# Kernel tuning notes

Measured on AMD Instinct MI355X. Metric: run time of the kernel, lower is better.

Reference implementation:

```python
import jax, jax.numpy as jnp
import numpy as np

N_A = 50000   # 'user' nodes
N_B = 50000   # 'item' nodes
E = 1000000   # edges per relation
IN, HID, OUT = 128, 128, 64


def setup_inputs() -> dict:
    key = jax.random.key(0)
    ks = jax.random.split(key, 24)
    def glorot(k, shape):
        scale = 1.0 / np.sqrt(shape[0])
        return jax.random.normal(k, shape, jnp.float32) * scale
    inp = {
        "feat_A": jax.random.normal(ks[0], (N_A, IN), jnp.float32),
        "feat_B": jax.random.normal(ks[1], (N_B, IN), jnp.float32),
        "rates_src": jax.random.randint(ks[2], (E,), 0, N_A, jnp.int32),
        "rates_dst": jax.random.randint(ks[3], (E,), 0, N_B, jnp.int32),
        "ratedby_src": jax.random.randint(ks[4], (E,), 0, N_B, jnp.int32),
        "ratedby_dst": jax.random.randint(ks[5], (E,), 0, N_A, jnp.int32),
        "follows_src": jax.random.randint(ks[6], (E,), 0, N_A, jnp.int32),
        "follows_dst": jax.random.randint(ks[7], (E,), 0, N_A, jnp.int32),
        "neg_src": jax.random.randint(ks[8], (E,), 0, N_A, jnp.int32),
        "neg_dst": jax.random.randint(ks[9], (E,), 0, N_B, jnp.int32),
        "W1_rates": glorot(ks[10], (IN, HID)),   "b1_rates": jnp.zeros((HID,), jnp.float32),
        "W1_ratedby": glorot(ks[11], (IN, HID)), "b1_ratedby": jnp.zeros((HID,), jnp.float32),
        "W1_follows": glorot(ks[12], (IN, HID)), "b1_follows": jnp.zeros((HID,), jnp.float32),
        "W2_rates": glorot(ks[13], (HID, OUT)),   "b2_rates": jnp.zeros((OUT,), jnp.float32),
        "W2_ratedby": glorot(ks[14], (HID, OUT)), "b2_ratedby": jnp.zeros((OUT,), jnp.float32),
        "W2_follows": glorot(ks[15], (HID, OUT)), "b2_follows": jnp.zeros((OUT,), jnp.float32),
    }
    return inp


def _graph_conv(x_src, W, b, src, dst, n_src, n_dst):
    # DGL GraphConv, norm='both': D_dst^{-1/2} A D_src^{-1/2} (X W) + b
    ones = jnp.ones(src.shape[0], x_src.dtype)
    deg_out = jnp.maximum(jax.ops.segment_sum(ones, src, num_segments=n_src), 1.0)
    deg_in = jnp.maximum(jax.ops.segment_sum(ones, dst, num_segments=n_dst), 1.0)
    h = (x_src * (deg_out ** -0.5)[:, None]) @ W          # [n_src, d_out]
    agg = jax.ops.segment_sum(h[src], dst, num_segments=n_dst)  # SpMM
    return agg * (deg_in ** -0.5)[:, None] + b


def reference(feat_A, feat_B,
              W1_rates, b1_rates, W1_ratedby, b1_ratedby, W1_follows, b1_follows,
              W2_rates, b2_rates, W2_ratedby, b2_ratedby, W2_follows, b2_follows,
              rates_src, rates_dst, ratedby_src, ratedby_dst,
              follows_src, follows_dst, neg_src, neg_dst):
    # --- RGCN layer 1 (HeteroGraphConv, aggregate='sum') ---
    hB = _graph_conv(feat_A, W1_rates, b1_rates, rates_src, rates_dst, N_A, N_B)
    hA = (_graph_conv(feat_B, W1_ratedby, b1_ratedby, ratedby_src, ratedby_dst, N_B, N_A)
          + _graph_conv(feat_A, W1_follows, b1_follows, follows_src, follows_dst, N_A, N_A))
    hA = jax.nn.relu(hA)
    hB = jax.nn.relu(hB)
    # --- RGCN layer 2 ---
    oB = _graph_conv(hA, W2_rates, b2_rates, rates_src, rates_dst, N_A, N_B)
    oA = (_graph_conv(hB, W2_ratedby, b2_ratedby, ratedby_src, ratedby_dst, N_B, N_A)
          + _graph_conv(hA, W2_follows, b2_follows, follows_src, follows_dst, N_A, N_A))
    # --- HeteroInnerProduct (u_dot_v on etype 'rates') for pos and neg graphs ---
    pos_score = jnp.sum(oA[rates_src] * oB[rates_dst], axis=1, keepdims=True)  # [E, 1]
    neg_score = jnp.sum(oA[neg_src] * oB[neg_dst], axis=1, keepdims=True)      # [E, 1]
    return pos_score, neg_score
```

## Files before the change

kernel.cpp:

```cpp
#include <hip/hip_runtime.h>
#include <hip/hip_fp16.h>
#include <cstddef>
#include <type_traits>

#define N_NODES 50000
#define E_EDGES 1000000
#define NBUCK 196
#define ACHUNK 3907
#define MTILES 3125

typedef _Float16 f16x8 __attribute__((ext_vector_type(8)));
typedef float f32x4 __attribute__((ext_vector_type(4)));

__global__ __launch_bounds__(256) void bucket_hist(const int* __restrict__ i0, const int* __restrict__ i1,
                                                   const int* __restrict__ i2, const int* __restrict__ i3,
                                                   const int* __restrict__ i4, const int* __restrict__ i5,
                                                   int* __restrict__ bhist) {
    int arr = blockIdx.y;
    const int* idx = arr == 0 ? i0 : arr == 1 ? i1 : arr == 2 ? i2
                   : arr == 3 ? i3 : arr == 4 ? i4 : i5;
    __shared__ int l[NBUCK];
    for (int b = threadIdx.x; b < NBUCK; b += 256) l[b] = 0;
    __syncthreads();
    int e0 = blockIdx.x * ACHUNK;
    int e1 = e0 + ACHUNK; if (e1 > E_EDGES) e1 = E_EDGES;
    for (int i = e0 + threadIdx.x; i < e1; i += 256)
        atomicAdd(&l[((unsigned)idx[i]) >> 8], 1);
    __syncthreads();
    for (int b = threadIdx.x; b < NBUCK; b += 256)
        if (l[b]) atomicAdd(&bhist[arr * NBUCK + b], l[b]);
}

__global__ void bucket_scan2(const int* __restrict__ bhist, int* __restrict__ gbase,
                             int* __restrict__ gcur) {
    int arr = blockIdx.x;
    if (threadIdx.x == 0) {
        int run = 0;
        for (int b = 0; b < NBUCK; b++) {
            gbase[arr * (NBUCK + 1) + b] = run;
            gcur[arr * NBUCK + b] = run;
            run += bhist[arr * NBUCK + b];
        }
        gbase[arr * (NBUCK + 1) + NBUCK] = run;
    }
}

__global__ __launch_bounds__(256) void binP(const int* __restrict__ s0, const int* __restrict__ d0,
                                            const int* __restrict__ s1, const int* __restrict__ d1,
                                            const int* __restrict__ s2, const int* __restrict__ d2,
                                            int* __restrict__ gcur, unsigned* __restrict__ pairs) {
    int rel = blockIdx.y;
    int arr = 2 * rel + 1;
    const int* src = rel == 0 ? s0 : rel == 1 ? s1 : s2;
    const int* dst = rel == 0 ? d0 : rel == 1 ? d1 : d2;
    int e0 = blockIdx.x * ACHUNK;
    int e1 = e0 + ACHUNK; if (e1 > E_EDGES) e1 = E_EDGES;
    __shared__ int lcnt[NBUCK];
    __shared__ int lbase[NBUCK];
    for (int b = threadIdx.x; b < NBUCK; b += 256) lcnt[b] = 0;
    __syncthreads();
    for (int i = e0 + threadIdx.x; i < e1; i += 256)
        atomicAdd(&lcnt[((unsigned)dst[i]) >> 8], 1);
    __syncthreads();
    for (int b = threadIdx.x; b < NBUCK; b += 256) {
        lbase[b] = lcnt[b] ? atomicAdd(&gcur[arr * NBUCK + b], lcnt[b]) : 0;
        lcnt[b] = 0;
    }
    __syncthreads();
    unsigned* pp = pairs + (size_t)rel * E_EDGES;
    for (int i = e0 + threadIdx.x; i < e1; i += 256) {
        int d = dst[i];
        int b = ((unsigned)d) >> 8;
        int p = lbase[b] + atomicAdd(&lcnt[b], 1);
        pp[p] = ((unsigned)(d & 255) << 16) | (unsigned)src[i];
    }
}

__global__ __launch_bounds__(256) void binS(const int* __restrict__ s0, const int* __restrict__ s1,
                                            const int* __restrict__ s2,
                                            int* __restrict__ gcur, unsigned char* __restrict__ sbytes) {
    int rel = blockIdx.y;
    int arr = 2 * rel;
    const int* src = rel == 0 ? s0 : rel == 1 ? s1 : s2;
    int e0 = blockIdx.x * ACHUNK;
    int e1 = e0 + ACHUNK; if (e1 > E_EDGES) e1 = E_EDGES;
    __shared__ int lcnt[NBUCK];
    __shared__ int lbase[NBUCK];
    for (int b = threadIdx.x; b < NBUCK; b += 256) lcnt[b] = 0;
    __syncthreads();
    for (int i = e0 + threadIdx.x; i < e1; i += 256)
        atomicAdd(&lcnt[((unsigned)src[i]) >> 8], 1);
    __syncthreads();
    for (int b = threadIdx.x; b < NBUCK; b += 256) {
        lbase[b] = lcnt[b] ? atomicAdd(&gcur[arr * NBUCK + b], lcnt[b]) : 0;
        lcnt[b] = 0;
    }
    __syncthreads();
    unsigned char* sb = sbytes + (size_t)rel * E_EDGES;
    for (int i = e0 + threadIdx.x; i < e1; i += 256) {
        int s = src[i];
        int b = ((unsigned)s) >> 8;
        int p = lbase[b] + atomicAdd(&lcnt[b], 1);
        sb[p] = (unsigned char)(s & 255);
    }
}

__global__ __launch_bounds__(256) void countS(const unsigned char* __restrict__ sbytes,
                                              const int* __restrict__ gbase,
                                              float* __restrict__ scales) {
    int rel = blockIdx.y, b = blockIdx.x;
    int arr = 2 * rel;
    int p0 = gbase[arr * (NBUCK + 1) + b];
    int p1 = gbase[arr * (NBUCK + 1) + b + 1];
    const unsigned char* sb = sbytes + (size_t)rel * E_EDGES;
    __shared__ int cnt[256];
    cnt[threadIdx.x] = 0;
    __syncthreads();
    for (int i = p0 + threadIdx.x; i < p1; i += 256)
        atomicAdd(&cnt[sb[i]], 1);
    __syncthreads();
    int node = b * 256 + threadIdx.x;
    if (node < N_NODES) {
        int c = cnt[threadIdx.x];
        if (c < 1) c = 1;
        scales[(size_t)arr * N_NODES + node] = 1.0f / sqrtf((float)c);
    }
}

__global__ __launch_bounds__(256) void fillB2(const unsigned* __restrict__ pairs,
                                              const int* __restrict__ gbase,
                                              int* __restrict__ row_ptr,
                                              float* __restrict__ scales,
                                              int* __restrict__ col) {
    int rel = blockIdx.y, b = blockIdx.x;
    int arr = 2 * rel + 1;
    int gb = gbase[arr * (NBUCK + 1) + b];
    int ge = gbase[arr * (NBUCK + 1) + b + 1];
    const unsigned* pp = pairs + (size_t)rel * E_EDGES;
    __shared__ int cnt[256];
    __shared__ int rowbase[256];
    __shared__ int wsum[4];
    int t = threadIdx.x;
    cnt[t] = 0;
    __syncthreads();
    for (int i = gb + t; i < ge; i += 256)
        atomicAdd(&cnt[pp[i] >> 16], 1);
    __syncthreads();
    int lane = t & 63, wid = t >> 6;
    int c0 = cnt[t];
    int v = c0;
#pragma unroll
    for (int o = 1; o < 64; o <<= 1) {
        int u = __shfl_up(v, o);
        if (lane >= o) v += u;
    }
    if (lane == 63) wsum[wid] = v;
    __syncthreads();
    int base = gb;
    for (int w = 0; w < wid; w++) base += wsum[w];
    int excl = base + v - c0;
    rowbase[t] = excl;
    int node = b * 256 + t;
    if (node <= N_NODES)
        row_ptr[(size_t)rel * (N_NODES + 1) + node] = excl;
    if (node < N_NODES) {
        int c = c0; if (c < 1) c = 1;
        scales[(size_t)arr * N_NODES + node] = 1.0f / sqrtf((float)c);
    }
    cnt[t] = 0;
    __syncthreads();
    int* cl = col + (size_t)rel * E_EDGES;
    for (int i = gb + t; i < ge; i += 256) {
        unsigned p = pp[i];
        int dl = p >> 16;
        int slot = rowbase[dl] + atomicAdd(&cnt[dl], 1);
        cl[slot] = (int)(p & 0xFFFFu);
    }
}

__global__ void w_cvt6(const float* __restrict__ w0, const float* __restrict__ w1,
                       const float* __restrict__ w2, const float* __restrict__ w3,
                       const float* __restrict__ w4, const float* __restrict__ w5,
                       __half* __restrict__ t0, __half* __restrict__ t1,
                       __half* __restrict__ t2, __half* __restrict__ t3,
                       __half* __restrict__ t4, __half* __restrict__ t5) {
    int m = blockIdx.y;
    const float* W = m == 0 ? w0 : m == 1 ? w1 : m == 2 ? w2 : m == 3 ? w3 : m == 4 ? w4 : w5;
    __half* Wt = m == 0 ? t0 : m == 1 ? t1 : m == 2 ? t2 : m == 3 ? t3 : m == 4 ? t4 : t5;
    int ncol = m < 3 ? 128 : 64;
    int tot = 128 * ncol;
    for (int i = blockIdx.x * blockDim.x + threadIdx.x; i < tot; i += gridDim.x * blockDim.x) {
        int n = i >> 7, k = i & 127;
        Wt[i] = __float2half(W[k * ncol + n]);
    }
}

template <int NCOL, typename XT>
__global__ __launch_bounds__(256) void gemm_mfma(const XT* __restrict__ X,
                                                 const float* __restrict__ sc,
                                                 const __half* __restrict__ Wt,
                                                 __half* __restrict__ T) {
    constexpr int NHALF = NCOL / 64;
    int gw = (blockIdx.x * blockDim.x + threadIdx.x) >> 6;
    int lane = threadIdx.x & 63;
    int half_id = gw % NHALF;
    int mstream = gw / NHALF;
    int nstreams = ((gridDim.x * blockDim.x) >> 6) / NHALF;
    int l15 = lane & 15, g = lane >> 4;

    f16x8 b[4][4];
    {
        const __half* wb = Wt + ((size_t)half_id * 64 + l15) * 128 + g * 8;
#pragma unroll
        for (int nt = 0; nt < 4; nt++)
#pragma unroll
            for (int kb = 0; kb < 4; kb++)
                b[nt][kb] = *(const f16x8*)(wb + nt * 16 * 128 + kb * 32);
    }

    for (int mt = mstream; mt < MTILES; mt += nstreams) {
        int m0 = mt * 16;
        f16x8 a[4];
        if constexpr (std::is_same<XT, float>::value) {
            const float* xr = X + (size_t)(m0 + l15) * 128 + g * 8;
#pragma unroll
            for (int kb = 0; kb < 4; kb++) {
                float4 u = *(const float4*)(xr + kb * 32);
                float4 v = *(const float4*)(xr + kb * 32 + 4);
                f16x8 t;
                t[0] = (_Float16)u.x; t[1] = (_Float16)u.y;
                t[2] = (_Float16)u.z; t[3] = (_Float16)u.w;
                t[4] = (_Float16)v.x; t[5] = (_Float16)v.y;
                t[6] = (_Float16)v.z; t[7] = (_Float16)v.w;
                a[kb] = t;
            }
        } else {
            const _Float16* xr = (const _Float16*)X + (size_t)(m0 + l15) * 128 + g * 8;
#pragma unroll
            for (int kb = 0; kb < 4; kb++)
                a[kb] = *(const f16x8*)(xr + kb * 32);
        }
        f32x4 acc[4];
#pragma unroll
        for (int nt = 0; nt < 4; nt++) acc[nt] = (f32x4){0.f, 0.f, 0.f, 0.f};
#pragma unroll
        for (int kb = 0; kb < 4; kb++)
#pragma unroll
            for (int nt = 0; nt < 4; nt++)
                acc[nt] = __builtin_amdgcn_mfma_f32_16x16x32_f16(a[kb], b[nt][kb], acc[nt], 0, 0, 0);
        int mrow = m0 + g * 4;
#pragma unroll
        for (int j = 0; j < 4; j++) {
            float sj = sc[mrow + j];
            __half* tj = T + (size_t)(mrow + j) * NCOL + half_id * 64 + l15;
            tj[0]  = __float2half(acc[0][j] * sj);
            tj[16] = __float2half(acc[1][j] * sj);
            tj[32] = __float2half(acc[2][j] * sj);
            tj[48] = __float2half(acc[3][j] * sj);
        }
    }
}

template <bool ACCUM, bool RELU>
__global__ __launch_bounds__(256) void spmm128(const int* __restrict__ rp,
                                               const int* __restrict__ col,
                                               const __half* __restrict__ T,
                                               const float* __restrict__ s_in,
                                               const float* __restrict__ bias,
                                               __half* __restrict__ outp, int nrows) {
    int wave = (blockIdx.x * blockDim.x + threadIdx.x) >> 6;
    int lane = threadIdx.x & 63;
    int rowA = wave * 2, rowB = rowA + 1;
    if (rowA >= nrows) return;
    const char* Tb = (const char*)T;
    unsigned loff = (unsigned)lane << 2;
#define LD128(c) __half22float2(*(const __half2*)(Tb + (((unsigned)(c) << 8) + loff)))
    int begA = rp[rowA], endA = rp[rowA + 1];
    int eB = endA, endB = (rowB < nrows) ? rp[rowB + 1] : endA;
    float axA = 0.f, ayA = 0.f, axB = 0.f, ayB = 0.f;
    int eA = begA;
    while (eA + 4 <= endA && eB + 4 <= endB) {
        int a0 = col[eA], a1 = col[eA+1], a2 = col[eA+2], a3 = col[eA+3];
        int b0 = col[eB], b1 = col[eB+1], b2 = col[eB+2], b3 = col[eB+3];
        float2 va0 = LD128(a0), va1 = LD128(a1), va2 = LD128(a2), va3 = LD128(a3);
        float2 vb0 = LD128(b0), vb1 = LD128(b1), vb2 = LD128(b2), vb3 = LD128(b3);
        axA += (va0.x + va1.x) + (va2.x + va3.x);
        ayA += (va0.y + va1.y) + (va2.y + va3.y);
        axB += (vb0.x + vb1.x) + (vb2.x + vb3.x);
        ayB += (vb0.y + vb1.y) + (vb2.y + vb3.y);
        eA += 4; eB += 4;
    }
    while (eA + 4 <= endA) {
        int a0 = col[eA], a1 = col[eA+1], a2 = col[eA+2], a3 = col[eA+3];
        float2 va0 = LD128(a0), va1 = LD128(a1), va2 = LD128(a2), va3 = LD128(a3);
        axA += (va0.x + va1.x) + (va2.x + va3.x);
        ayA += (va0.y + va1.y) + (va2.y + va3.y);
        eA += 4;
    }
    while (eB + 4 <= endB) {
        int b0 = col[eB], b1 = col[eB+1], b2 = col[eB+2], b3 = col[eB+3];
        float2 vb0 = LD128(b0), vb1 = LD128(b1), vb2 = LD128(b2), vb3 = LD128(b3);
        axB += (vb0.x + vb1.x) + (vb2.x + vb3.x);
        ayB += (vb0.y + vb1.y) + (vb2.y + vb3.y);
        eB += 4;
    }
    while (eA < endA && eB < endB) {
        float2 va = LD128(col[eA]), vb = LD128(col[eB]);
        axA += va.x; ayA += va.y; axB += vb.x; ayB += vb.y;
        eA++; eB++;
    }
    for (; eA < endA; eA++) { float2 v = LD128(col[eA]); axA += v.x; ayA += v.y; }
    for (; eB < endB; eB++) { float2 v = LD128(col[eB]); axB += v.x; ayB += v.y; }
#undef LD128
    float bx = bias[2 * lane], by = bias[2 * lane + 1];
    {
        float s = s_in[rowA];
        __half2* po = (__half2*)(outp + (size_t)rowA * 128 + 2 * lane);
        float ox = fmaf(axA, s, bx), oy = fmaf(ayA, s, by);
        if constexpr (ACCUM) { float2 p = __half22float2(*po); ox += p.x; oy += p.y; }
        if constexpr (RELU) { ox = fmaxf(ox, 0.f); oy = fmaxf(oy, 0.f); }
        *po = __floats2half2_rn(ox, oy);
    }
    if (rowB < nrows) {
        float s = s_in[rowB];
        __half2* po = (__half2*)(outp + (size_t)rowB * 128 + 2 * lane);
        float ox = fmaf(axB, s, bx), oy = fmaf(ayB, s, by);
        if constexpr (ACCUM) { float2 p = __half22float2(*po); ox += p.x; oy += p.y; }
        if constexpr (RELU) { ox = fmaxf(ox, 0.f); oy = fmaxf(oy, 0.f); }
        *po = __floats2half2_rn(ox, oy);
    }
}

template <bool ACCUM>
__global__ __launch_bounds__(256) void spmm64(const int* __restrict__ rp,
                                              const int* __restrict__ col,
                                              const __half* __restrict__ T,
                                              const float* __restrict__ s_in,
                                              const float* __restrict__ bias,
                                              __half* __restrict__ outp, int nrows) {
    int g = (blockIdx.x * blockDim.x + threadIdx.x) >> 5;
    int l2 = threadIdx.x & 31;
    int rowA = g * 2, rowB = rowA + 1;
    if (rowA >= nrows) return;
    const char* Tb = (const char*)T;
    unsigned loff = (unsigned)l2 << 2;
#define LD64(c) __half22float2(*(const __half2*)(Tb + (((unsigned)(c) << 7) + loff)))
    int begA = rp[rowA], endA = rp[rowA + 1];
    int eB = endA, endB = (rowB < nrows) ? rp[rowB + 1] : endA;
    float axA = 0.f, ayA = 0.f, axB = 0.f, ayB = 0.f;
    int eA = begA;
    while (eA + 4 <= endA && eB + 4 <= endB) {
        int a0 = col[eA], a1 = col[eA+1], a2 = col[eA+2], a3 = col[eA+3];
        int b0 = col[eB], b1 = col[eB+1], b2 = col[eB+2], b3 = col[eB+3];
        float2 va0 = LD64(a0), va1 = LD64(a1), va2 = LD64(a2), va3 = LD64(a3);
        float2 vb0 = LD64(b0), vb1 = LD64(b1), vb2 = LD64(b2), vb3 = LD64(b3);
        axA += (va0.x + va1.x) + (va2.x + va3.x);
        ayA += (va0.y + va1.y) + (va2.y + va3.y);
        axB += (vb0.x + vb1.x) + (vb2.x + vb3.x);
        ayB += (vb0.y + vb1.y) + (vb2.y + vb3.y);
        eA += 4; eB += 4;
    }
    while (eA + 4 <= endA) {
        int a0 = col[eA], a1 = col[eA+1], a2 = col[eA+2], a3 = col[eA+3];
        float2 va0 = LD64(a0), va1 = LD64(a1), va2 = LD64(a2), va3 = LD64(a3);
        axA += (va0.x + va1.x) + (va2.x + va3.x);
        ayA += (va0.y + va1.y) + (va2.y + va3.y);
        eA += 4;
    }
    while (eB + 4 <= endB) {
        int b0 = col[eB], b1 = col[eB+1], b2 = col[eB+2], b3 = col[eB+3];
        float2 vb0 = LD64(b0), vb1 = LD64(b1), vb2 = LD64(b2), vb3 = LD64(b3);
        axB += (vb0.x + vb1.x) + (vb2.x + vb3.x);
        ayB += (vb0.y + vb1.y) + (vb2.y + vb3.y);
        eB += 4;
    }
    while (eA < endA && eB < endB) {
        float2 va = LD64(col[eA]), vb = LD64(col[eB]);
        axA += va.x; ayA += va.y; axB += vb.x; ayB += vb.y;
        eA++; eB++;
    }
    for (; eA < endA; eA++) { float2 v = LD64(col[eA]); axA += v.x; ayA += v.y; }
    for (; eB < endB; eB++) { float2 v = LD64(col[eB]); axB += v.x; ayB += v.y; }
#undef LD64
    float bx = bias[2 * l2], by = bias[2 * l2 + 1];
    {
        float s = s_in[rowA];
        __half2* po = (__half2*)(outp + (size_t)rowA * 64 + 2 * l2);
        float ox = fmaf(axA, s, bx), oy = fmaf(ayA, s, by);
        if constexpr (ACCUM) { float2 p = __half22float2(*po); ox += p.x; oy += p.y; }
        *po = __floats2half2_rn(ox, oy);
    }
    if (rowB < nrows) {
        float s = s_in[rowB];
        __half2* po = (__half2*)(outp + (size_t)rowB * 64 + 2 * l2);
        float ox = fmaf(axB, s, bx), oy = fmaf(ayB, s, by);
        if constexpr (ACCUM) { float2 p = __half22float2(*po); ox += p.x; oy += p.y; }
        *po = __floats2half2_rn(ox, oy);
    }
}

__global__ __launch_bounds__(256) void score_kernel(const __half* __restrict__ oA,
                                                    const __half* __restrict__ oB,
                                                    const int* __restrict__ src,
                                                    const int* __restrict__ dst,
                                                    float* __restrict__ out, int n) {
    int g = (blockIdx.x * blockDim.x + threadIdx.x) >> 4;
    int l = threadIdx.x & 15;
    int ng = (gridDim.x * blockDim.x) >> 4;
    const char* A = (const char*)oA;
    const char* B = (const char*)oB;
    unsigned loff = (unsigned)l << 3;
    for (int e0 = g * 2; e0 < n; e0 += ng * 2) {
        int e1 = e0 + 1;
        int s0 = src[e0], d0 = dst[e0], s1 = src[e1], d1 = dst[e1];
        union { uint2 u; __half2 h[2]; } a0, b0, a1, b1;
        a0.u = *(const uint2*)(A + (((unsigned)s0 << 7) + loff));
        b0.u = *(const uint2*)(B + (((unsigned)d0 << 7) + loff));
        a1.u = *(const uint2*)(A + (((unsigned)s1 << 7) + loff));
        b1.u = *(const uint2*)(B + (((unsigned)d1 << 7) + loff));
        float2 fa, fb;
        fa = __half22float2(a0.h[0]); fb = __half22float2(b0.h[0]);
        float p0 = fa.x * fb.x + fa.y * fb.y;
        fa = __half22float2(a0.h[1]); fb = __half22float2(b0.h[1]);
        p0 += fa.x * fb.x + fa.y * fb.y;
        fa = __half22float2(a1.h[0]); fb = __half22float2(b1.h[0]);
        float p1 = fa.x * fb.x + fa.y * fb.y;
        fa = __half22float2(a1.h[1]); fb = __half22float2(b1.h[1]);
        p1 += fa.x * fb.x + fa.y * fb.y;
        p0 += __shfl_xor(p0, 8); p1 += __shfl_xor(p1, 8);
        p0 += __shfl_xor(p0, 4); p1 += __shfl_xor(p1, 4);
        p0 += __shfl_xor(p0, 2); p1 += __shfl_xor(p1, 2);
        p0 += __shfl_xor(p0, 1); p1 += __shfl_xor(p1, 1);
        if (l == 0) { out[e0] = p0; out[e1] = p1; }
    }
}

extern "C" void kernel_launch(void* const* d_in, const int* in_sizes, int n_in,
                              void* d_out, int out_size, void* d_ws, size_t ws_size,
                              hipStream_t stream) {
    const float* feat_A     = (const float*)d_in[0];
    const float* feat_B     = (const float*)d_in[1];
    const int* rates_src    = (const int*)d_in[2];
    const int* rates_dst    = (const int*)d_in[3];
    const int* ratedby_src  = (const int*)d_in[4];
    const int* ratedby_dst  = (const int*)d_in[5];
    const int* follows_src  = (const int*)d_in[6];
    const int* follows_dst  = (const int*)d_in[7];
    const int* neg_src      = (const int*)d_in[8];
    const int* neg_dst      = (const int*)d_in[9];
    const float* W1_rates   = (const float*)d_in[10];
    const float* b1_rates   = (const float*)d_in[11];
    const float* W1_ratedby = (const float*)d_in[12];
    const float* b1_ratedby = (const float*)d_in[13];
    const float* W1_follows = (const float*)d_in[14];
    const float* b1_follows = (const float*)d_in[15];
    const float* W2_rates   = (const float*)d_in[16];
    const float* b2_rates   = (const float*)d_in[17];
    const float* W2_ratedby = (const float*)d_in[18];
    const float* b2_ratedby = (const float*)d_in[19];
    const float* W2_follows = (const float*)d_in[20];
    const float* b2_follows = (const float*)d_in[21];

    const int N = N_NODES, E = E_EDGES;

    char* ws = (char*)d_ws;
    size_t off = 0;
    auto alloc = [&](size_t bytes) -> void* {
        void* p = ws + off;
        off += (bytes + 255) & ~(size_t)255;
        return p;
    };
    float* scales = (float*)alloc((size_t)6 * N * 4);
    int* row_ptr  = (int*)alloc((size_t)3 * (N + 1) * 4);
    int* bhist    = (int*)alloc((size_t)6 * NBUCK * 4);
    int* gbase    = (int*)alloc((size_t)6 * (NBUCK + 1) * 4);
    int* gcur     = (int*)alloc((size_t)6 * NBUCK * 4);
    int* col      = (int*)alloc((size_t)3 * E * 4);
    __half* T     = (__half*)alloc((size_t)N * 128 * 4);
    __half* hA    = (__half*)alloc((size_t)N * 128 * 2);
    __half* hB    = (__half*)alloc((size_t)N * 128 * 2);
    __half* oA    = (__half*)alloc((size_t)N * 64 * 2);
    __half* oB    = (__half*)alloc((size_t)N * 64 * 2);
    __half* Wt    = (__half*)alloc((size_t)(3 * 128 * 128 + 3 * 128 * 64) * 2);
    (void)ws_size;
    __half* Wt1_rates   = Wt;
    __half* Wt1_ratedby = Wt + 16384;
    __half* Wt1_follows = Wt + 32768;
    __half* Wt2_rates   = Wt + 49152;
    __half* Wt2_ratedby = Wt + 57344;
    __half* Wt2_follows = Wt + 65536;
    unsigned* pairs = (unsigned*)T;
    unsigned char* sbytes = (unsigned char*)(pairs + (size_t)3 * E);

    w_cvt6<<<dim3(16, 6), 256, 0, stream>>>(W1_rates, W1_ratedby, W1_follows,
                                            W2_rates, W2_ratedby, W2_follows,
                                            Wt1_rates, Wt1_ratedby, Wt1_follows,
                                            Wt2_rates, Wt2_ratedby, Wt2_follows);
    hipMemsetAsync(bhist, 0, (size_t)6 * NBUCK * 4, stream);
    bucket_hist<<<dim3(256, 6), 256, 0, stream>>>(rates_src, rates_dst, ratedby_src,
                                                  ratedby_dst, follows_src, follows_dst,
                                                  bhist);
    bucket_scan2<<<6, 64, 0, stream>>>(bhist, gbase, gcur);
    binP<<<dim3(256, 3), 256, 0, stream>>>(rates_src, rates_dst, ratedby_src,
                                           ratedby_dst, follows_src, follows_dst,
                                           gcur, pairs);
    binS<<<dim3(256, 3), 256, 0, stream>>>(rates_src, ratedby_src, follows_src,
                                           gcur, sbytes);
    countS<<<dim3(NBUCK, 3), 256, 0, stream>>>(sbytes, gbase, scales);
    fillB2<<<dim3(NBUCK, 3), 256, 0, stream>>>(pairs, gbase, row_ptr, scales, col);

    const int* rp0 = row_ptr;                 const int* cl0 = col;
    const int* rp1 = row_ptr + (N + 1);       const int* cl1 = col + E;
    const int* rp2 = row_ptr + 2 * (N + 1);   const int* cl2 = col + 2 * (size_t)E;
    const float* s_rates_out   = scales;
    const float* s_rates_in    = scales + N;
    const float* s_ratedby_out = scales + 2 * N;
    const float* s_ratedby_in  = scales + 3 * N;
    const float* s_follows_out = scales + 4 * N;
    const float* s_follows_in  = scales + 5 * N;

    const int GB128 = 384;
    const int GB64  = 256;
    const int SB128 = (N / 2 + 3) / 4;
    const int SB64  = (N / 2 + 7) / 8;

    gemm_mfma<128, float><<<GB128, 256, 0, stream>>>(feat_A, s_rates_out, Wt1_rates, T);
    spmm128<false, true><<<SB128, 256, 0, stream>>>(rp0, cl0, T, s_rates_in,
                                                    b1_rates, hB, N);
    gemm_mfma<128, float><<<GB128, 256, 0, stream>>>(feat_B, s_ratedby_out, Wt1_ratedby, T);
    spmm128<false, false><<<SB128, 256, 0, stream>>>(rp1, cl1, T, s_ratedby_in,
                                                     b1_ratedby, hA, N);
    gemm_mfma<128, float><<<GB128, 256, 0, stream>>>(feat_A, s_follows_out, Wt1_follows, T);
    spmm128<true, true><<<SB128, 256, 0, stream>>>(rp2, cl2, T, s_follows_in,
                                                   b1_follows, hA, N);

    gemm_mfma<64, __half><<<GB64, 256, 0, stream>>>(hA, s_rates_out, Wt2_rates, T);
    spmm64<false><<<SB64, 256, 0, stream>>>(rp0, cl0, T, s_rates_in, b2_rates, oB, N);
    gemm_mfma<64, __half><<<GB64, 256, 0, stream>>>(hB, s_ratedby_out, Wt2_ratedby, T);
    spmm64<false><<<SB64, 256, 0, stream>>>(rp1, cl1, T, s_ratedby_in, b2_ratedby, oA, N);
    gemm_mfma<64, __half><<<GB64, 256, 0, stream>>>(hA, s_follows_out, Wt2_follows, T);
    spmm64<true><<<SB64, 256, 0, stream>>>(rp2, cl2, T, s_follows_in, b2_follows, oA, N);

    float* outp = (float*)d_out;
    score_kernel<<<8192, 256, 0, stream>>>(oA, oB, rates_src, rates_dst, outp, E);
    score_kernel<<<8192, 256, 0, stream>>>(oA, oB, neg_src, neg_dst, outp + E, E);
}
```

Before: 444.8 us.

## Fuse graph preprocessing and per-relation GEMM/SpMM launches into batched kernels

Folds the many preprocessing launches (weight convert, histogram, scan, two binning passes, count and fill) into four kernels. The histogram now writes per-block partials, so the memset and the global atomics go away, and the bucket scan becomes a parallel wave scan instead of a single-thread loop. The three per-relation GEMMs and SpMMs of each layer are batched into one launch each, with a separate T buffer per relation, and the two score passes become one kernel. This cuts launch count and serialization and lets independent relations fill the GPU together, at the cost of extra workspace memory and an in-kernel combine of relations that share an output row.

```diff
diff --git a/kernel.cpp b/kernel.cpp
--- a/kernel.cpp
+++ b/kernel.cpp
@@ -8,204 +8,207 @@
 #define NBUCK 196
 #define ACHUNK 3907
 #define MTILES 3125
+#define HB 96
+#define HCHUNK 10417
+#define GB1 384
+#define GB2 256
 
 typedef _Float16 f16x8 __attribute__((ext_vector_type(8)));
 typedef float f32x4 __attribute__((ext_vector_type(4)));
 
-__global__ __launch_bounds__(256) void bucket_hist(const int* __restrict__ i0, const int* __restrict__ i1,
-                                                   const int* __restrict__ i2, const int* __restrict__ i3,
-                                                   const int* __restrict__ i4, const int* __restrict__ i5,
-                                                   int* __restrict__ bhist) {
-    int arr = blockIdx.y;
-    const int* idx = arr == 0 ? i0 : arr == 1 ? i1 : arr == 2 ? i2
-                   : arr == 3 ? i3 : arr == 4 ? i4 : i5;
-    __shared__ int l[NBUCK];
-    for (int b = threadIdx.x; b < NBUCK; b += 256) l[b] = 0;
+__global__ __launch_bounds__(256) void fused0(
+        const float* __restrict__ w0, const float* __restrict__ w1,
+        const float* __restrict__ w2, const float* __restrict__ w3,
+        const float* __restrict__ w4, const float* __restrict__ w5,
+        __half* __restrict__ Wt,
+        const int* __restrict__ rs, const int* __restrict__ rd,
+        const int* __restrict__ bs, const int* __restrict__ bd,
+        const int* __restrict__ fs, const int* __restrict__ fd,
+        int* __restrict__ bphist) {
+    int bx = blockIdx.x;
+    if (bx < 6 * HB) {
+        __shared__ int l[NBUCK];
+        int arr = bx / HB, blk = bx % HB;
+        const int* idx = arr == 0 ? rs : arr == 1 ? rd : arr == 2 ? bs
+                       : arr == 3 ? bd : arr == 4 ? fs : fd;
+        for (int b = threadIdx.x; b < NBUCK; b += 256) l[b] = 0;
+        __syncthreads();
+        int e0 = blk * HCHUNK;
+        int e1 = e0 + HCHUNK; if (e1 > E_EDGES) e1 = E_EDGES;
+        for (int i = e0 + threadIdx.x; i < e1; i += 256)
+            atomicAdd(&l[((unsigned)idx[i]) >> 8], 1);
+        __syncthreads();
+        int* dst = bphist + (size_t)(arr * HB + blk) * NBUCK;
+        for (int b = threadIdx.x; b < NBUCK; b += 256) dst[b] = l[b];
+        return;
+    }
+    bx -= 6 * HB;
+    int m = bx / 16, part = bx % 16;
+    const float* W = m == 0 ? w0 : m == 1 ? w1 : m == 2 ? w2 : m == 3 ? w3 : m == 4 ? w4 : w5;
+    __half* Tt = Wt + (m < 3 ? m * 16384 : 49152 + (m - 3) * 8192);
+    int ncol = m < 3 ? 128 : 64;
+    int tot = 128 * ncol;
+    for (int i = part * 256 + threadIdx.x; i < tot; i += 16 * 256) {
+        int n = i >> 7, k = i & 127;
+        Tt[i] = __float2half(W[k * ncol + n]);
+    }
+}
+
+__global__ void bucket_scan_par(const int* __restrict__ bphist, int* __restrict__ gbase,
+                                int* __restrict__ gcur) {
+    int arr = blockIdx.x;
+    int t = threadIdx.x;
+    int c = 0;
+    if (t < NBUCK) {
+        const int* p = bphist + (size_t)arr * HB * NBUCK + t;
+#pragma unroll 8
+        for (int blk = 0; blk < HB; blk++) c += p[(size_t)blk * NBUCK];
+    }
+    int lane = t & 63, wid = t >> 6;
+    __shared__ int wsum[4];
+    int v = c;
+#pragma unroll
+    for (int o = 1; o < 64; o <<= 1) { int u = __shfl_up(v, o); if (lane >= o) v += u; }
+    if (lane == 63) wsum[wid] = v;
     __syncthreads();
+    int base = 0;
+    for (int ww = 0; ww < wid; ww++) base += wsum[ww];
+    int excl = base + v - c;
+    if (t < NBUCK) {
+        gbase[arr * (NBUCK + 1) + t] = excl;
+        gcur[arr * NBUCK + t] = excl;
+    }
+    if (t == 255) gbase[arr * (NBUCK + 1) + NBUCK] = base + v;
+}
+
+__global__ __launch_bounds__(256) void fused_bin(
+        const int* __restrict__ rs, const int* __restrict__ rd,
+        const int* __restrict__ bs, const int* __restrict__ bd,
+        const int* __restrict__ fs, const int* __restrict__ fd,
+        int* __restrict__ gcur, unsigned* __restrict__ pairs,
+        unsigned char* __restrict__ sbytes) {
+    int y = blockIdx.y;
+    __shared__ int lcnt[NBUCK];
+    __shared__ int lbase[NBUCK];
     int e0 = blockIdx.x * ACHUNK;
     int e1 = e0 + ACHUNK; if (e1 > E_EDGES) e1 = E_EDGES;
-    for (int i = e0 + threadIdx.x; i < e1; i += 256)
-        atomicAdd(&l[((unsigned)idx[i]) >> 8], 1);
-    __syncthreads();
-    for (int b = threadIdx.x; b < NBUCK; b += 256)
-        if (l[b]) atomicAdd(&bhist[arr * NBUCK + b], l[b]);
-}
-
-__global__ void bucket_scan2(const int* __restrict__ bhist, int* __restrict__ gbase,
-                             int* __restrict__ gcur) {
-    int arr = blockIdx.x;
-    if (threadIdx.x == 0) {
-        int run = 0;
-        for (int b = 0; b < NBUCK; b++) {
-            gbase[arr * (NBUCK + 1) + b] = run;
-            gcur[arr * NBUCK + b] = run;
-            run += bhist[arr * NBUCK + b];
-        }
-        gbase[arr * (NBUCK + 1) + NBUCK] = run;
-    }
-}
-
-__global__ __launch_bounds__(256) void binP(const int* __restrict__ s0, const int* __restrict__ d0,
-                                            const int* __restrict__ s1, const int* __restrict__ d1,
-                                            const int* __restrict__ s2, const int* __restrict__ d2,
-                                            int* __restrict__ gcur, unsigned* __restrict__ pairs) {
-    int rel = blockIdx.y;
-    int arr = 2 * rel + 1;
-    const int* src = rel == 0 ? s0 : rel == 1 ? s1 : s2;
-    const int* dst = rel == 0 ? d0 : rel == 1 ? d1 : d2;
-    int e0 = blockIdx.x * ACHUNK;
-    int e1 = e0 + ACHUNK; if (e1 > E_EDGES) e1 = E_EDGES;
-    __shared__ int lcnt[NBUCK];
-    __shared__ int lbase[NBUCK];
     for (int b = threadIdx.x; b < NBUCK; b += 256) lcnt[b] = 0;
     __syncthreads();
-    for (int i = e0 + threadIdx.x; i < e1; i += 256)
-        atomicAdd(&lcnt[((unsigned)dst[i]) >> 8], 1);
-    __syncthreads();
-    for (int b = threadIdx.x; b < NBUCK; b += 256) {
-        lbase[b] = lcnt[b] ? atomicAdd(&gcur[arr * NBUCK + b], lcnt[b]) : 0;
-        lcnt[b] = 0;
-    }
-    __syncthreads();
-    unsigned* pp = pairs + (size_t)rel * E_EDGES;
-    for (int i = e0 + threadIdx.x; i < e1; i += 256) {
-        int d = dst[i];
-        int b = ((unsigned)d) >> 8;
-        int p = lbase[b] + atomicAdd(&lcnt[b], 1);
-        pp[p] = ((unsigned)(d & 255) << 16) | (unsigned)src[i];
-    }
-}
-
-__global__ __launch_bounds__(256) void binS(const int* __restrict__ s0, const int* __restrict__ s1,
-                                            const int* __restrict__ s2,
-                                            int* __restrict__ gcur, unsigned char* __restrict__ sbytes) {
-    int rel = blockIdx.y;
-    int arr = 2 * rel;
-    const int* src = rel == 0 ? s0 : rel == 1 ? s1 : s2;
-    int e0 = blockIdx.x * ACHUNK;
-    int e1 = e0 + ACHUNK; if (e1 > E_EDGES) e1 = E_EDGES;
-    __shared__ int lcnt[NBUCK];
-    __shared__ int lbase[NBUCK];
-    for (int b = threadIdx.x; b < NBUCK; b += 256) lcnt[b] = 0;
-    __syncthreads();
-    for (int i = e0 + threadIdx.x; i < e1; i += 256)
-        atomicAdd(&lcnt[((unsigned)src[i]) >> 8], 1);
-    __syncthreads();
-    for (int b = threadIdx.x; b < NBUCK; b += 256) {
-        lbase[b] = lcnt[b] ? atomicAdd(&gcur[arr * NBUCK + b], lcnt[b]) : 0;
-        lcnt[b] = 0;
-    }
-    __syncthreads();
-    unsigned char* sb = sbytes + (size_t)rel * E_EDGES;
-    for (int i = e0 + threadIdx.x; i < e1; i += 256) {
-        int s = src[i];
-        int b = ((unsigned)s) >> 8;
-        int p = lbase[b] + atomicAdd(&lcnt[b], 1);
-        sb[p] = (unsigned char)(s & 255);
-    }
-}
-
-__global__ __launch_bounds__(256) void countS(const unsigned char* __restrict__ sbytes,
-                                              const int* __restrict__ gbase,
-                                              float* __restrict__ scales) {
-    int rel = blockIdx.y, b = blockIdx.x;
-    int arr = 2 * rel;
-    int p0 = gbase[arr * (NBUCK + 1) + b];
-    int p1 = gbase[arr * (NBUCK + 1) + b + 1];
-    const unsigned char* sb = sbytes + (size_t)rel * E_EDGES;
-    __shared__ int cnt[256];
-    cnt[threadIdx.x] = 0;
-    __syncthreads();
-    for (int i = p0 + threadIdx.x; i < p1; i += 256)
-        atomicAdd(&cnt[sb[i]], 1);
-    __syncthreads();
-    int node = b * 256 + threadIdx.x;
-    if (node < N_NODES) {
-        int c = cnt[threadIdx.x];
-        if (c < 1) c = 1;
-        scales[(size_t)arr * N_NODES + node] = 1.0f / sqrtf((float)c);
-    }
-}
-
-__global__ __launch_bounds__(256) void fillB2(const unsigned* __restrict__ pairs,
-                                              const int* __restrict__ gbase,
-                                              int* __restrict__ row_ptr,
-                                              float* __restrict__ scales,
-                                              int* __restrict__ col) {
-    int rel = blockIdx.y, b = blockIdx.x;
-    int arr = 2 * rel + 1;
-    int gb = gbase[arr * (NBUCK + 1) + b];
-    int ge = gbase[arr * (NBUCK + 1) + b + 1];
-    const unsigned* pp = pairs + (size_t)rel * E_EDGES;
+    if (y < 3) {
+        int rel = y, arr = 2 * rel + 1;
+        const int* src = rel == 0 ? rs : rel == 1 ? bs : fs;
+        const int* dst = rel == 0 ? rd : rel == 1 ? bd : fd;
+        for (int i = e0 + threadIdx.x; i < e1; i += 256)
+            atomicAdd(&lcnt[((unsigned)dst[i]) >> 8], 1);
+        __syncthreads();
+        for (int b = threadIdx.x; b < NBUCK; b += 256) {
+            lbase[b] = lcnt[b] ? atomicAdd(&gcur[arr * NBUCK + b], lcnt[b]) : 0;
+            lcnt[b] = 0;
+        }
+        __syncthreads();
+        unsigned* pp = pairs + (size_t)rel * E_EDGES;
+        for (int i = e0 + threadIdx.x; i < e1; i += 256) {
+            int d = dst[i];
+            int b = ((unsigned)d) >> 8;
+            int p = lbase[b] + atomicAdd(&lcnt[b], 1);
+            pp[p] = ((unsigned)(d & 255) << 16) | (unsigned)src[i];
+        }
+    } else {
+        int rel = y - 3, arr = 2 * rel;
+        const int* src = rel == 0 ? rs : rel == 1 ? bs : fs;
+        for (int i = e0 + threadIdx.x; i < e1; i += 256)
+            atomicAdd(&lcnt[((unsigned)src[i]) >> 8], 1);
+        __syncthreads();
+        for (int b = threadIdx.x; b < NBUCK; b += 256) {
+            lbase[b] = lcnt[b] ? atomicAdd(&gcur[arr * NBUCK + b], lcnt[b]) : 0;
+            lcnt[b] = 0;
+        }
+        __syncthreads();
+        unsigned char* sb = sbytes + (size_t)rel * E_EDGES;
+        for (int i = e0 + threadIdx.x; i < e1; i += 256) {
+            int s = src[i];
+            int b = ((unsigned)s) >> 8;
+            int p = lbase[b] + atomicAdd(&lcnt[b], 1);
+            sb[p] = (unsigned char)(s & 255);
+        }
+    }
+}
+
+__global__ __launch_bounds__(256) void fused_finish(
+        const unsigned* __restrict__ pairs, const unsigned char* __restrict__ sbytes,
+        const int* __restrict__ gbase, int* __restrict__ row_ptr,
+        float* __restrict__ scales, int* __restrict__ col) {
+    int y = blockIdx.y, b = blockIdx.x, t = threadIdx.x;
     __shared__ int cnt[256];
     __shared__ int rowbase[256];
     __shared__ int wsum[4];
-    int t = threadIdx.x;
-    cnt[t] = 0;
-    __syncthreads();
-    for (int i = gb + t; i < ge; i += 256)
-        atomicAdd(&cnt[pp[i] >> 16], 1);
-    __syncthreads();
-    int lane = t & 63, wid = t >> 6;
-    int c0 = cnt[t];
-    int v = c0;
-#pragma unroll
-    for (int o = 1; o < 64; o <<= 1) {
-        int u = __shfl_up(v, o);
-        if (lane >= o) v += u;
-    }
-    if (lane == 63) wsum[wid] = v;
-    __syncthreads();
-    int base = gb;
-    for (int w = 0; w < wid; w++) base += wsum[w];
-    int excl = base + v - c0;
-    rowbase[t] = excl;
-    int node = b * 256 + t;
-    if (node <= N_NODES)
-        row_ptr[(size_t)rel * (N_NODES + 1) + node] = excl;
-    if (node < N_NODES) {
-        int c = c0; if (c < 1) c = 1;
-        scales[(size_t)arr * N_NODES + node] = 1.0f / sqrtf((float)c);
-    }
-    cnt[t] = 0;
-    __syncthreads();
-    int* cl = col + (size_t)rel * E_EDGES;
-    for (int i = gb + t; i < ge; i += 256) {
-        unsigned p = pp[i];
-        int dl = p >> 16;
-        int slot = rowbase[dl] + atomicAdd(&cnt[dl], 1);
-        cl[slot] = (int)(p & 0xFFFFu);
-    }
-}
-
-__global__ void w_cvt6(const float* __restrict__ w0, const float* __restrict__ w1,
-                       const float* __restrict__ w2, const float* __restrict__ w3,
-                       const float* __restrict__ w4, const float* __restrict__ w5,
-                       __half* __restrict__ t0, __half* __restrict__ t1,
-                       __half* __restrict__ t2, __half* __restrict__ t3,
-                       __half* __restrict__ t4, __half* __restrict__ t5) {
-    int m = blockIdx.y;
-    const float* W = m == 0 ? w0 : m == 1 ? w1 : m == 2 ? w2 : m == 3 ? w3 : m == 4 ? w4 : w5;
-    __half* Wt = m == 0 ? t0 : m == 1 ? t1 : m == 2 ? t2 : m == 3 ? t3 : m == 4 ? t4 : t5;
-    int ncol = m < 3 ? 128 : 64;
-    int tot = 128 * ncol;
-    for (int i = blockIdx.x * blockDim.x + threadIdx.x; i < tot; i += gridDim.x * blockDim.x) {
-        int n = i >> 7, k = i & 127;
-        Wt[i] = __float2half(W[k * ncol + n]);
+    if (y < 3) {
+        int rel = y, arr = 2 * rel;
+        int p0 = gbase[arr * (NBUCK + 1) + b];
+        int p1 = gbase[arr * (NBUCK + 1) + b + 1];
+        const unsigned char* sb = sbytes + (size_t)rel * E_EDGES;
+        cnt[t] = 0;
+        __syncthreads();
+        for (int i = p0 + t; i < p1; i += 256)
+            atomicAdd(&cnt[sb[i]], 1);
+        __syncthreads();
+        int node = b * 256 + t;
+        if (node < N_NODES) {
+            int c = cnt[t]; if (c < 1) c = 1;
+            scales[(size_t)arr * N_NODES + node] = 1.0f / sqrtf((float)c);
+        }
+    } else {
+        int rel = y - 3, arr = 2 * rel + 1;
+        int gb = gbase[arr * (NBUCK + 1) + b];
+        int ge = gbase[arr * (NBUCK + 1) + b + 1];
+        const unsigned* pp = pairs + (size_t)rel * E_EDGES;
+        cnt[t] = 0;
+        __syncthreads();
+        for (int i = gb + t; i < ge; i += 256)
+            atomicAdd(&cnt[pp[i] >> 16], 1);
+        __syncthreads();
+        int lane = t & 63, wid = t >> 6;
+        int c0 = cnt[t];
+        int v = c0;
+#pragma unroll
+        for (int o = 1; o < 64; o <<= 1) { int u = __shfl_up(v, o); if (lane >= o) v += u; }
+        if (lane == 63) wsum[wid] = v;
+        __syncthreads();
+        int base = gb;
+        for (int w = 0; w < wid; w++) base += wsum[w];
+        int excl = base + v - c0;
+        rowbase[t] = excl;
+        int node = b * 256 + t;
+        if (node <= N_NODES)
+            row_ptr[(size_t)rel * (N_NODES + 1) + node] = excl;
+        if (node < N_NODES) {
+            int c = c0; if (c < 1) c = 1;
+            scales[(size_t)arr * N_NODES + node] = 1.0f / sqrtf((float)c);
+        }
+        cnt[t] = 0;
+        __syncthreads();
+        int* cl = col + (size_t)rel * E_EDGES;
+        for (int i = gb + t; i < ge; i += 256) {
+            unsigned p = pp[i];
+            int dl = p >> 16;
+            int slot = rowbase[dl] + atomicAdd(&cnt[dl], 1);
+            cl[slot] = (int)(p & 0xFFFFu);
+        }
     }
 }
 
 template <int NCOL, typename XT>
-__global__ __launch_bounds__(256) void gemm_mfma(const XT* __restrict__ X,
-                                                 const float* __restrict__ sc,
-                                                 const __half* __restrict__ Wt,
-                                                 __half* __restrict__ T) {
+__device__ __forceinline__ void gemm_body(const XT* __restrict__ X,
+                                          const float* __restrict__ sc,
+                                          const __half* __restrict__ Wt,
+                                          __half* __restrict__ T,
+                                          int bxr, int nblocks) {
     constexpr int NHALF = NCOL / 64;
-    int gw = (blockIdx.x * blockDim.x + threadIdx.x) >> 6;
+    int gw = bxr * 4 + ((int)threadIdx.x >> 6);
     int lane = threadIdx.x & 63;
     int half_id = gw % NHALF;
     int mstream = gw / NHALF;
-    int nstreams = ((gridDim.x * blockDim.x) >> 6) / NHALF;
+    int nstreams = nblocks * 4 / NHALF;
     int l15 = lane & 15, g = lane >> 4;
 
     f16x8 b[4][4];
@@ -261,178 +264,270 @@
     }
 }
 
-template <bool ACCUM, bool RELU>
-__global__ __launch_bounds__(256) void spmm128(const int* __restrict__ rp,
-                                               const int* __restrict__ col,
-                                               const __half* __restrict__ T,
-                                               const float* __restrict__ s_in,
-                                               const float* __restrict__ bias,
-                                               __half* __restrict__ outp, int nrows) {
-    int wave = (blockIdx.x * blockDim.x + threadIdx.x) >> 6;
+__global__ __launch_bounds__(256) void gemm_l1(const float* __restrict__ fA,
+                                               const float* __restrict__ fB,
+                                               const float* __restrict__ scales,
+                                               const __half* __restrict__ Wt,
+                                               __half* __restrict__ T012) {
+    int rel = blockIdx.x / GB1, bxr = blockIdx.x % GB1;
+    const float* X = (rel == 1) ? fB : fA;
+    const float* sc = scales + (rel == 0 ? 0 : rel == 1 ? 2 * N_NODES : 4 * N_NODES);
+    const __half* W = Wt + rel * 16384;
+    __half* T = T012 + (size_t)rel * N_NODES * 128;
+    gemm_body<128, float>(X, sc, W, T, bxr, GB1);
+}
+
+__global__ __launch_bounds__(256) void gemm_l2(const __half* __restrict__ hA,
+                                               const __half* __restrict__ hB,
+                                               const float* __restrict__ scales,
+                                               const __half* __restrict__ Wt,
+                                               __half* __restrict__ Tp) {
+    int rel = blockIdx.x / GB2, bxr = blockIdx.x % GB2;
+    const __half* X = (rel == 1) ? hB : hA;
+    const float* sc = scales + (rel == 0 ? 0 : rel == 1 ? 2 * N_NODES : 4 * N_NODES);
+    const __half* W = Wt + 49152 + rel * 8192;
+    __half* T = Tp + (size_t)rel * N_NODES * 64;
+    gemm_body<64, __half>(X, sc, W, T, bxr, GB2);
+}
+
+__global__ __launch_bounds__(256) void spmm_l1(
+        const int* __restrict__ row_ptr, const int* __restrict__ col,
+        const __half* __restrict__ T012, const float* __restrict__ scales,
+        const float* __restrict__ b1r, const float* __restrict__ b1rb,
+        const float* __restrict__ b1f,
+        __half* __restrict__ hB, __half* __restrict__ hA) {
+    int w = (blockIdx.x * blockDim.x + threadIdx.x) >> 6;
     int lane = threadIdx.x & 63;
-    int rowA = wave * 2, rowB = rowA + 1;
-    if (rowA >= nrows) return;
-    const char* Tb = (const char*)T;
     unsigned loff = (unsigned)lane << 2;
-#define LD128(c) __half22float2(*(const __half2*)(Tb + (((unsigned)(c) << 8) + loff)))
-    int begA = rp[rowA], endA = rp[rowA + 1];
-    int eB = endA, endB = (rowB < nrows) ? rp[rowB + 1] : endA;
-    float axA = 0.f, ayA = 0.f, axB = 0.f, ayB = 0.f;
-    int eA = begA;
-    while (eA + 4 <= endA && eB + 4 <= endB) {
-        int a0 = col[eA], a1 = col[eA+1], a2 = col[eA+2], a3 = col[eA+3];
-        int b0 = col[eB], b1 = col[eB+1], b2 = col[eB+2], b3 = col[eB+3];
-        float2 va0 = LD128(a0), va1 = LD128(a1), va2 = LD128(a2), va3 = LD128(a3);
-        float2 vb0 = LD128(b0), vb1 = LD128(b1), vb2 = LD128(b2), vb3 = LD128(b3);
-        axA += (va0.x + va1.x) + (va2.x + va3.x);
-        ayA += (va0.y + va1.y) + (va2.y + va3.y);
-        axB += (vb0.x + vb1.x) + (vb2.x + vb3.x);
-        ayB += (vb0.y + vb1.y) + (vb2.y + vb3.y);
-        eA += 4; eB += 4;
-    }
-    while (eA + 4 <= endA) {
-        int a0 = col[eA], a1 = col[eA+1], a2 = col[eA+2], a3 = col[eA+3];
-        float2 va0 = LD128(a0), va1 = LD128(a1), va2 = LD128(a2), va3 = LD128(a3);
-        axA += (va0.x + va1.x) + (va2.x + va3.x);
-        ayA += (va0.y + va1.y) + (va2.y + va3.y);
-        eA += 4;
-    }
-    while (eB + 4 <= endB) {
-        int b0 = col[eB], b1 = col[eB+1], b2 = col[eB+2], b3 = col[eB+3];
-        float2 vb0 = LD128(b0), vb1 = LD128(b1), vb2 = LD128(b2), vb3 = LD128(b3);
-        axB += (vb0.x + vb1.x) + (vb2.x + vb3.x);
-        ayB += (vb0.y + vb1.y) + (vb2.y + vb3.y);
-        eB += 4;
-    }
-    while (eA < endA && eB < endB) {
-        float2 va = LD128(col[eA]), vb = LD128(col[eB]);
-        axA += va.x; ayA += va.y; axB += vb.x; ayB += vb.y;
-        eA++; eB++;
-    }
-    for (; eA < endA; eA++) { float2 v = LD128(col[eA]); axA += v.x; ayA += v.y; }
-    for (; eB < endB; eB++) { float2 v = LD128(col[eB]); axB += v.x; ayB += v.y; }
-#undef LD128
-    float bx = bias[2 * lane], by = bias[2 * lane + 1];
-    {
-        float s = s_in[rowA];
-        __half2* po = (__half2*)(outp + (size_t)rowA * 128 + 2 * lane);
-        float ox = fmaf(axA, s, bx), oy = fmaf(ayA, s, by);
-        if constexpr (ACCUM) { float2 p = __half22float2(*po); ox += p.x; oy += p.y; }
-        if constexpr (RELU) { ox = fmaxf(ox, 0.f); oy = fmaxf(oy, 0.f); }
-        *po = __floats2half2_rn(ox, oy);
-    }
-    if (rowB < nrows) {
-        float s = s_in[rowB];
-        __half2* po = (__half2*)(outp + (size_t)rowB * 128 + 2 * lane);
-        float ox = fmaf(axB, s, bx), oy = fmaf(ayB, s, by);
-        if constexpr (ACCUM) { float2 p = __half22float2(*po); ox += p.x; oy += p.y; }
-        if constexpr (RELU) { ox = fmaxf(ox, 0.f); oy = fmaxf(oy, 0.f); }
-        *po = __floats2half2_rn(ox, oy);
-    }
-}
-
-template <bool ACCUM>
-__global__ __launch_bounds__(256) void spmm64(const int* __restrict__ rp,
-                                              const int* __restrict__ col,
-                                              const __half* __restrict__ T,
-                                              const float* __restrict__ s_in,
-                                              const float* __restrict__ bias,
-                                              __half* __restrict__ outp, int nrows) {
+    const char* T0 = (const char*)T012;
+    const char* T1 = T0 + (size_t)N_NODES * 256;
+    const char* T2 = T1 + (size_t)N_NODES * 256;
+#define LDT(B, c) __half22float2(*(const __half2*)((B) + (((unsigned)(c) << 8) + loff)))
+    if (w < N_NODES / 2) {
+        const int* cl = col;
+        int rowA = w * 2, rowB = rowA + 1;
+        int eA = row_ptr[rowA], EA = row_ptr[rowA + 1];
+        int eB = EA, EB = row_ptr[rowB + 1];
+        float axA = 0.f, ayA = 0.f, axB = 0.f, ayB = 0.f;
+        while (eA + 4 <= EA && eB + 4 <= EB) {
+            int a0 = cl[eA], a1 = cl[eA+1], a2 = cl[eA+2], a3 = cl[eA+3];
+            int b0 = cl[eB], b1 = cl[eB+1], b2 = cl[eB+2], b3 = cl[eB+3];
+            float2 v0 = LDT(T0, a0), v1 = LDT(T0, a1), v2 = LDT(T0, a2), v3 = LDT(T0, a3);
+            float2 u0 = LDT(T0, b0), u1 = LDT(T0, b1), u2 = LDT(T0, b2), u3 = LDT(T0, b3);
+            axA += (v0.x + v1.x) + (v2.x + v3.x); ayA += (v0.y + v1.y) + (v2.y + v3.y);
+            axB += (u0.x + u1.x) + (u2.x + u3.x); ayB += (u0.y + u1.y) + (u2.y + u3.y);
+            eA += 4; eB += 4;
+        }
+        while (eA + 4 <= EA) {
+            int a0 = cl[eA], a1 = cl[eA+1], a2 = cl[eA+2], a3 = cl[eA+3];
+            float2 v0 = LDT(T0, a0), v1 = LDT(T0, a1), v2 = LDT(T0, a2), v3 = LDT(T0, a3);
+            axA += (v0.x + v1.x) + (v2.x + v3.x); ayA += (v0.y + v1.y) + (v2.y + v3.y);
+            eA += 4;
+        }
+        while (eB + 4 <= EB) {
+            int b0 = cl[eB], b1 = cl[eB+1], b2 = cl[eB+2], b3 = cl[eB+3];
+            float2 u0 = LDT(T0, b0), u1 = LDT(T0, b1), u2 = LDT(T0, b2), u3 = LDT(T0, b3);
+            axB += (u0.x + u1.x) + (u2.x + u3.x); ayB += (u0.y + u1.y) + (u2.y + u3.y);
+            eB += 4;
+        }
+        while (eA < EA && eB < EB) {
+            float2 v = LDT(T0, cl[eA]), u = LDT(T0, cl[eB]);
+            axA += v.x; ayA += v.y; axB += u.x; ayB += u.y;
+            eA++; eB++;
+        }
+        for (; eA < EA; eA++) { float2 v = LDT(T0, cl[eA]); axA += v.x; ayA += v.y; }
+        for (; eB < EB; eB++) { float2 v = LDT(T0, cl[eB]); axB += v.x; ayB += v.y; }
+        float bx = b1r[2 * lane], by = b1r[2 * lane + 1];
+        float sA = scales[N_NODES + rowA], sB = scales[N_NODES + rowB];
+        float ox = fmaxf(fmaf(axA, sA, bx), 0.f), oy = fmaxf(fmaf(ayA, sA, by), 0.f);
+        *(__half2*)(hB + (size_t)rowA * 128 + 2 * lane) = __floats2half2_rn(ox, oy);
+        ox = fmaxf(fmaf(axB, sB, bx), 0.f); oy = fmaxf(fmaf(ayB, sB, by), 0.f);
+        *(__half2*)(hB + (size_t)rowB * 128 + 2 * lane) = __floats2half2_rn(ox, oy);
+    } else {
+        int r = w - N_NODES / 2;
+        const int* rp1 = row_ptr + (N_NODES + 1);
+        const int* rp2 = row_ptr + 2 * (N_NODES + 1);
+        const int* cl1 = col + E_EDGES;
+        const int* cl2 = col + 2 * (size_t)E_EDGES;
+        int e1 = rp1[r], E1 = rp1[r + 1];
+        int e2 = rp2[r], E2 = rp2[r + 1];
+        float a1x = 0.f, a1y = 0.f, a2x = 0.f, a2y = 0.f;
+        while (e1 + 4 <= E1 && e2 + 4 <= E2) {
+            int a0 = cl1[e1], a1 = cl1[e1+1], a2 = cl1[e1+2], a3 = cl1[e1+3];
+            int b0 = cl2[e2], b1 = cl2[e2+1], b2 = cl2[e2+2], b3 = cl2[e2+3];
+            float2 v0 = LDT(T1, a0), v1 = LDT(T1, a1), v2 = LDT(T1, a2), v3 = LDT(T1, a3);
+            float2 u0 = LDT(T2, b0), u1 = LDT(T2, b1), u2 = LDT(T2, b2), u3 = LDT(T2, b3);
+            a1x += (v0.x + v1.x) + (v2.x + v3.x); a1y += (v0.y + v1.y) + (v2.y + v3.y);
+            a2x += (u0.x + u1.x) + (u2.x + u3.x); a2y += (u0.y + u1.y) + (u2.y + u3.y);
+            e1 += 4; e2 += 4;
+        }
+        while (e1 + 4 <= E1) {
+            int a0 = cl1[e1], a1 = cl1[e1+1], a2 = cl1[e1+2], a3 = cl1[e1+3];
+            float2 v0 = LDT(T1, a0), v1 = LDT(T1, a1), v2 = LDT(T1, a2), v3 = LDT(T1, a3);
+            a1x += (v0.x + v1.x) + (v2.x + v3.x); a1y += (v0.y + v1.y) + (v2.y + v3.y);
+            e1 += 4;
+        }
+        while (e2 + 4 <= E2) {
+            int b0 = cl2[e2], b1 = cl2[e2+1], b2 = cl2[e2+2], b3 = cl2[e2+3];
+            float2 u0 = LDT(T2, b0), u1 = LDT(T2, b1), u2 = LDT(T2, b2), u3 = LDT(T2, b3);
+            a2x += (u0.x + u1.x) + (u2.x + u3.x); a2y += (u0.y + u1.y) + (u2.y + u3.y);
+            e2 += 4;
+        }
+        while (e1 < E1 && e2 < E2) {
+            float2 v = LDT(T1, cl1[e1]), u = LDT(T2, cl2[e2]);
+            a1x += v.x; a1y += v.y; a2x += u.x; a2y += u.y;
+            e1++; e2++;
+        }
+        for (; e1 < E1; e1++) { float2 v = LDT(T1, cl1[e1]); a1x += v.x; a1y += v.y; }
+        for (; e2 < E2; e2++) { float2 v = LDT(T2, cl2[e2]); a2x += v.x; a2y += v.y; }
+        float s1 = scales[3 * N_NODES + r], s2 = scales[5 * N_NODES + r];
+        float ox = a1x * s1 + a2x * s2 + b1rb[2 * lane] + b1f[2 * lane];
+        float oy = a1y * s1 + a2y * s2 + b1rb[2 * lane + 1] + b1f[2 * lane + 1];
+        ox = fmaxf(ox, 0.f); oy = fmaxf(oy, 0.f);
+        *(__half2*)(hA + (size_t)r * 128 + 2 * lane) = __floats2half2_rn(ox, oy);
+    }
+#undef LDT
+}
+
+__global__ __launch_bounds__(256) void spmm_l2(
+        const int* __restrict__ row_ptr, const int* __restrict__ col,
+        const __half* __restrict__ Tp, const float* __restrict__ scales,
+        const float* __restrict__ b2r, const float* __restrict__ b2rb,
+        const float* __restrict__ b2f,
+        __half* __restrict__ oB, __half* __restrict__ oA) {
     int g = (blockIdx.x * blockDim.x + threadIdx.x) >> 5;
     int l2 = threadIdx.x & 31;
-    int rowA = g * 2, rowB = rowA + 1;
-    if (rowA >= nrows) return;
-    const char* Tb = (const char*)T;
     unsigned loff = (unsigned)l2 << 2;
-#define LD64(c) __half22float2(*(const __half2*)(Tb + (((unsigned)(c) << 7) + loff)))
-    int begA = rp[rowA], endA = rp[rowA + 1];
-    int eB = endA, endB = (rowB < nrows) ? rp[rowB + 1] : endA;
-    float axA = 0.f, ayA = 0.f, axB = 0.f, ayB = 0.f;
-    int eA = begA;
-    while (eA + 4 <= endA && eB + 4 <= endB) {
-        int a0 = col[eA], a1 = col[eA+1], a2 = col[eA+2], a3 = col[eA+3];
-        int b0 = col[eB], b1 = col[eB+1], b2 = col[eB+2], b3 = col[eB+3];
-        float2 va0 = LD64(a0), va1 = LD64(a1), va2 = LD64(a2), va3 = LD64(a3);
-        float2 vb0 = LD64(b0), vb1 = LD64(b1), vb2 = LD64(b2), vb3 = LD64(b3);
-        axA += (va0.x + va1.x) + (va2.x + va3.x);
-        ayA += (va0.y + va1.y) + (va2.y + va3.y);
-        axB += (vb0.x + vb1.x) + (vb2.x + vb3.x);
-        ayB += (vb0.y + vb1.y) + (vb2.y + vb3.y);
-        eA += 4; eB += 4;
-    }
-    while (eA + 4 <= endA) {
-        int a0 = col[eA], a1 = col[eA+1], a2 = col[eA+2], a3 = col[eA+3];
-        float2 va0 = LD64(a0), va1 = LD64(a1), va2 = LD64(a2), va3 = LD64(a3);
-        axA += (va0.x + va1.x) + (va2.x + va3.x);
-        ayA += (va0.y + va1.y) + (va2.y + va3.y);
-        eA += 4;
-    }
-    while (eB + 4 <= endB) {
-        int b0 = col[eB], b1 = col[eB+1], b2 = col[eB+2], b3 = col[eB+3];
-        float2 vb0 = LD64(b0), vb1 = LD64(b1), vb2 = LD64(b2), vb3 = LD64(b3);
-        axB += (vb0.x + vb1.x) + (vb2.x + vb3.x);
-        ayB += (vb0.y + vb1.y) + (vb2.y + vb3.y);
-        eB += 4;
-    }
-    while (eA < endA && eB < endB) {
-        float2 va = LD64(col[eA]), vb = LD64(col[eB]);
-        axA += va.x; ayA += va.y; axB += vb.x; ayB += vb.y;
-        eA++; eB++;
-    }
-    for (; eA < endA; eA++) { float2 v = LD64(col[eA]); axA += v.x; ayA += v.y; }
-    for (; eB < endB; eB++) { float2 v = LD64(col[eB]); axB += v.x; ayB += v.y; }
-#undef LD64
-    float bx = bias[2 * l2], by = bias[2 * l2 + 1];
-    {
-        float s = s_in[rowA];
-        __half2* po = (__half2*)(outp + (size_t)rowA * 64 + 2 * l2);
-        float ox = fmaf(axA, s, bx), oy = fmaf(ayA, s, by);
-        if constexpr (ACCUM) { float2 p = __half22float2(*po); ox += p.x; oy += p.y; }
-        *po = __floats2half2_rn(ox, oy);
-    }
-    if (rowB < nrows) {
-        float s = s_in[rowB];
-        __half2* po = (__half2*)(outp + (size_t)rowB * 64 + 2 * l2);
-        float ox = fmaf(axB, s, bx), oy = fmaf(ayB, s, by);
-        if constexpr (ACCUM) { float2 p = __half22float2(*po); ox += p.x; oy += p.y; }
-        *po = __floats2half2_rn(ox, oy);
-    }
-}
-
-__global__ __launch_bounds__(256) void score_kernel(const __half* __restrict__ oA,
-                                                    const __half* __restrict__ oB,
-                                                    const int* __restrict__ src,
-                                                    const int* __restrict__ dst,
-                                                    float* __restrict__ out, int n) {
+    const char* T0 = (const char*)Tp;
+    const char* T1 = T0 + (size_t)N_NODES * 128;
+    const char* T2 = T1 + (size_t)N_NODES * 128;
+#define LDT(B, c) __half22float2(*(const __half2*)((B) + (((unsigned)(c) << 7) + loff)))
+    if (g < N_NODES / 2) {
+        const int* cl = col;
+        int rowA = g * 2, rowB = rowA + 1;
+        int eA = row_ptr[rowA], EA = row_ptr[rowA + 1];
+        int eB = EA, EB = row_ptr[rowB + 1];
+        float axA = 0.f, ayA = 0.f, axB = 0.f, ayB = 0.f;
+        while (eA + 4 <= EA && eB + 4 <= EB) {
+            int a0 = cl[eA], a1 = cl[eA+1], a2 = cl[eA+2], a3 = cl[eA+3];
+            int b0 = cl[eB], b1 = cl[eB+1], b2 = cl[eB+2], b3 = cl[eB+3];
+            float2 v0 = LDT(T0, a0), v1 = LDT(T0, a1), v2 = LDT(T0, a2), v3 = LDT(T0, a3);
+            float2 u0 = LDT(T0, b0), u1 = LDT(T0, b1), u2 = LDT(T0, b2), u3 = LDT(T0, b3);
+            axA += (v0.x + v1.x) + (v2.x + v3.x); ayA += (v0.y + v1.y) + (v2.y + v3.y);
+            axB += (u0.x + u1.x) + (u2.x + u3.x); ayB += (u0.y + u1.y) + (u2.y + u3.y);
+            eA += 4; eB += 4;
+        }
+        while (eA + 4 <= EA) {
+            int a0 = cl[eA], a1 = cl[eA+1], a2 = cl[eA+2], a3 = cl[eA+3];
+            float2 v0 = LDT(T0, a0), v1 = LDT(T0, a1), v2 = LDT(T0, a2), v3 = LDT(T0, a3);
+            axA += (v0.x + v1.x) + (v2.x + v3.x); ayA += (v0.y + v1.y) + (v2.y + v3.y);
+            eA += 4;
+        }
+        while (eB + 4 <= EB) {
+            int b0 = cl[eB], b1 = cl[eB+1], b2 = cl[eB+2], b3 = cl[eB+3];
+            float2 u0 = LDT(T0, b0), u1 = LDT(T0, b1), u2 = LDT(T0, b2), u3 = LDT(T0, b3);
+            axB += (u0.x + u1.x) + (u2.x + u3.x); ayB += (u0.y + u1.y) + (u2.y + u3.y);
+            eB += 4;
+        }
+        while (eA < EA && eB < EB) {
+            float2 v = LDT(T0, cl[eA]), u = LDT(T0, cl[eB]);
+            axA += v.x; ayA += v.y; axB += u.x; ayB += u.y;
+            eA++; eB++;
+        }
+        for (; eA < EA; eA++) { float2 v = LDT(T0, cl[eA]); axA += v.x; ayA += v.y; }
+        for (; eB < EB; eB++) { float2 v = LDT(T0, cl[eB]); axB += v.x; ayB += v.y; }
+        float bx = b2r[2 * l2], by = b2r[2 * l2 + 1];
+        float sA = scales[N_NODES + rowA], sB = scales[N_NODES + rowB];
+        *(__half2*)(oB + (size_t)rowA * 64 + 2 * l2) =
+            __floats2half2_rn(fmaf(axA, sA, bx), fmaf(ayA, sA, by));
+        *(__half2*)(oB + (size_t)rowB * 64 + 2 * l2) =
+            __floats2half2_rn(fmaf(axB, sB, bx), fmaf(ayB, sB, by));
+    } else {
+        int r = g - N_NODES / 2;
+        const int* rp1 = row_ptr + (N_NODES + 1);
+        const int* rp2 = row_ptr + 2 * (N_NODES + 1);
+        const int* cl1 = col + E_EDGES;
+        const int* cl2 = col + 2 * (size_t)E_EDGES;
+        int e1 = rp1[r], E1 = rp1[r + 1];
+        int e2 = rp2[r], E2 = rp2[r + 1];
+        float a1x = 0.f, a1y = 0.f, a2x = 0.f, a2y = 0.f;
+        while (e1 + 4 <= E1 && e2 + 4 <= E2) {
+            int a0 = cl1[e1], a1 = cl1[e1+1], a2 = cl1[e1+2], a3 = cl1[e1+3];
+            int b0 = cl2[e2], b1 = cl2[e2+1], b2 = cl2[e2+2], b3 = cl2[e2+3];
+            float2 v0 = LDT(T1, a0), v1 = LDT(T1, a1), v2 = LDT(T1, a2), v3 = LDT(T1, a3);
+            float2 u0 = LDT(T2, b0), u1 = LDT(T2, b1), u2 = LDT(T2, b2), u3 = LDT(T2, b3);
+            a1x += (v0.x + v1.x) + (v2.x + v3.x); a1y += (v0.y + v1.y) + (v2.y + v3.y);
+            a2x += (u0.x + u1.x) + (u2.x + u3.x); a2y += (u0.y + u1.y) + (u2.y + u3.y);
+            e1 += 4; e2 += 4;
+        }
+        while (e1 + 4 <= E1) {
+            int a0 = cl1[e1], a1 = cl1[e1+1], a2 = cl1[e1+2], a3 = cl1[e1+3];
+            float2 v0 = LDT(T1, a0), v1 = LDT(T1, a1), v2 = LDT(T1, a2), v3 = LDT(T1, a3);
+            a1x += (v0.x + v1.x) + (v2.x + v3.x); a1y += (v0.y + v1.y) + (v2.y + v3.y);
+            e1 += 4;
+        }
+        while (e2 + 4 <= E2) {
+            int b0 = cl2[e2], b1 = cl2[e2+1], b2 = cl2[e2+2], b3 = cl2[e2+3];
+            float2 u0 = LDT(T2, b0), u1 = LDT(T2, b1), u2 = LDT(T2, b2), u3 = LDT(T2, b3);
+            a2x += (u0.x + u1.x) + (u2.x + u3.x); a2y += (u0.y + u1.y) + (u2.y + u3.y);
+            e2 += 4;
+        }
+        while (e1 < E1 && e2 < E2) {
+            float2 v = LDT(T1, cl1[e1]), u = LDT(T2, cl2[e2]);
+            a1x += v.x; a1y += v.y; a2x += u.x; a2y += u.y;
+            e1++; e2++;
+        }
+        for (; e1 < E1; e1++) { float2 v = LDT(T1, cl1[e1]); a1x += v.x; a1y += v.y; }
+        for (; e2 < E2; e2++) { float2 v = LDT(T2, cl2[e2]); a2x += v.x; a2y += v.y; }
+        float s1 = scales[3 * N_NODES + r], s2 = scales[5 * N_NODES + r];
+        float ox = a1x * s1 + a2x * s2 + b2rb[2 * l2] + b2f[2 * l2];
+        float oy = a1y * s1 + a2y * s2 + b2rb[2 * l2 + 1] + b2f[2 * l2 + 1];
+        *(__half2*)(oA + (size_t)r * 64 + 2 * l2) = __floats2half2_rn(ox, oy);
+    }
+#undef LDT
+}
+
+__global__ __launch_bounds__(256) void score2(const __half* __restrict__ oA,
+                                              const __half* __restrict__ oB,
+                                              const int* __restrict__ ps,
+                                              const int* __restrict__ pd,
+                                              const int* __restrict__ ns,
+                                              const int* __restrict__ nd,
+                                              float* __restrict__ out) {
     int g = (blockIdx.x * blockDim.x + threadIdx.x) >> 4;
     int l = threadIdx.x & 15;
     int ng = (gridDim.x * blockDim.x) >> 4;
     const char* A = (const char*)oA;
     const char* B = (const char*)oB;
     unsigned loff = (unsigned)l << 3;
-    for (int e0 = g * 2; e0 < n; e0 += ng * 2) {
-        int e1 = e0 + 1;
-        int s0 = src[e0], d0 = dst[e0], s1 = src[e1], d1 = dst[e1];
-        union { uint2 u; __half2 h[2]; } a0, b0, a1, b1;
-        a0.u = *(const uint2*)(A + (((unsigned)s0 << 7) + loff));
-        b0.u = *(const uint2*)(B + (((unsigned)d0 << 7) + loff));
-        a1.u = *(const uint2*)(A + (((unsigned)s1 << 7) + loff));
-        b1.u = *(const uint2*)(B + (((unsigned)d1 << 7) + loff));
-        float2 fa, fb;
-        fa = __half22float2(a0.h[0]); fb = __half22float2(b0.h[0]);
-        float p0 = fa.x * fb.x + fa.y * fb.y;
-        fa = __half22float2(a0.h[1]); fb = __half22float2(b0.h[1]);
-        p0 += fa.x * fb.x + fa.y * fb.y;
-        fa = __half22float2(a1.h[0]); fb = __half22float2(b1.h[0]);
-        float p1 = fa.x * fb.x + fa.y * fb.y;
-        fa = __half22float2(a1.h[1]); fb = __half22float2(b1.h[1]);
-        p1 += fa.x * fb.x + fa.y * fb.y;
-        p0 += __shfl_xor(p0, 8); p1 += __shfl_xor(p1, 8);
-        p0 += __shfl_xor(p0, 4); p1 += __shfl_xor(p1, 4);
-        p0 += __shfl_xor(p0, 2); p1 += __shfl_xor(p1, 2);
-        p0 += __shfl_xor(p0, 1); p1 += __shfl_xor(p1, 1);
-        if (l == 0) { out[e0] = p0; out[e1] = p1; }
-    }
+#define SCORE_LOOP(SRC, DST, OUT)                                               \
+    for (int e0 = g * 2; e0 < E_EDGES; e0 += ng * 2) {                          \
+        int e1 = e0 + 1;                                                        \
+        int s0 = SRC[e0], d0 = DST[e0], s1 = SRC[e1], d1 = DST[e1];             \
+        union { uint2 u; __half2 h[2]; } a0, b0, a1, b1;                        \
+        a0.u = *(const uint2*)(A + (((unsigned)s0 << 7) + loff));               \
+        b0.u = *(const uint2*)(B + (((unsigned)d0 << 7) + loff));               \
+        a1.u = *(const uint2*)(A + (((unsigned)s1 << 7) + loff));               \
+        b1.u = *(const uint2*)(B + (((unsigned)d1 << 7) + loff));               \
+        float2 fa, fb;                                                          \
+        fa = __half22float2(a0.h[0]); fb = __half22float2(b0.h[0]);             \
+        float p0 = fa.x * fb.x + fa.y * fb.y;                                   \
+        fa = __half22float2(a0.h[1]); fb = __half22float2(b0.h[1]);             \
+        p0 += fa.x * fb.x + fa.y * fb.y;                                        \
+        fa = __half22float2(a1.h[0]); fb = __half22float2(b1.h[0]);             \
+        float p1 = fa.x * fb.x + fa.y * fb.y;                                   \
+        fa = __half22float2(a1.h[1]); fb = __half22float2(b1.h[1]);             \
+        p1 += fa.x * fb.x + fa.y * fb.y;                                        \
+        p0 += __shfl_xor(p0, 8); p1 += __shfl_xor(p1, 8);                       \
+        p0 += __shfl_xor(p0, 4); p1 += __shfl_xor(p1, 4);                       \
+        p0 += __shfl_xor(p0, 2); p1 += __shfl_xor(p1, 2);                       \
+        p0 += __shfl_xor(p0, 1); p1 += __shfl_xor(p1, 1);                       \
+        if (l == 0) { OUT[e0] = p0; OUT[e1] = p1; }                             \
+    }
+    SCORE_LOOP(ps, pd, out)
+    float* outn = out + E_EDGES;
+    SCORE_LOOP(ns, nd, outn)
+#undef SCORE_LOOP
 }
 
 extern "C" void kernel_launch(void* const* d_in, const int* in_sizes, int n_in,
@@ -472,76 +567,41 @@
     };
     float* scales = (float*)alloc((size_t)6 * N * 4);
     int* row_ptr  = (int*)alloc((size_t)3 * (N + 1) * 4);
-    int* bhist    = (int*)alloc((size_t)6 * NBUCK * 4);
+    int* bphist   = (int*)alloc((size_t)6 * HB * NBUCK * 4);
     int* gbase    = (int*)alloc((size_t)6 * (NBUCK + 1) * 4);
     int* gcur     = (int*)alloc((size_t)6 * NBUCK * 4);
     int* col      = (int*)alloc((size_t)3 * E * 4);
-    __half* T     = (__half*)alloc((size_t)N * 128 * 4);
+    unsigned* pairs = (unsigned*)alloc((size_t)3 * E * 4);
+    unsigned char* sbytes = (unsigned char*)alloc((size_t)3 * E);
+    __half* T012  = (__half*)alloc((size_t)3 * N * 128 * 2);
+    __half* Tp    = (__half*)alloc((size_t)3 * N * 64 * 2);
     __half* hA    = (__half*)alloc((size_t)N * 128 * 2);
     __half* hB    = (__half*)alloc((size_t)N * 128 * 2);
     __half* oA    = (__half*)alloc((size_t)N * 64 * 2);
     __half* oB    = (__half*)alloc((size_t)N * 64 * 2);
     __half* Wt    = (__half*)alloc((size_t)(3 * 128 * 128 + 3 * 128 * 64) * 2);
     (void)ws_size;
-    __half* Wt1_rates   = Wt;
-    __half* Wt1_ratedby = Wt + 16384;
-    __half* Wt1_follows = Wt + 32768;
-    __half* Wt2_rates   = Wt + 49152;
-    __half* Wt2_ratedby = Wt + 57344;
-    __half* Wt2_follows = Wt + 65536;
-    unsigned* pairs = (unsigned*)T;
-    unsigned char* sbytes = (unsigned char*)(pairs + (size_t)3 * E);
-
-    w_cvt6<<<dim3(16, 6), 256, 0, stream>>>(W1_rates, W1_ratedby, W1_follows,
-                                            W2_rates, W2_ratedby, W2_follows,
-                                            Wt1_rates, Wt1_ratedby, Wt1_follows,
-                                            Wt2_rates, Wt2_ratedby, Wt2_follows);
-    hipMemsetAsync(bhist, 0, (size_t)6 * NBUCK * 4, stream);
-    bucket_hist<<<dim3(256, 6), 256, 0, stream>>>(rates_src, rates_dst, ratedby_src,
-                                                  ratedby_dst, follows_src, follows_dst,
-                                                  bhist);
-    bucket_scan2<<<6, 64, 0, stream>>>(bhist, gbase, gcur);
-    binP<<<dim3(256, 3), 256, 0, stream>>>(rates_src, rates_dst, ratedby_src,
-                                           ratedby_dst, follows_src, follows_dst,
-                                           gcur, pairs);
-    binS<<<dim3(256, 3), 256, 0, stream>>>(rates_src, ratedby_src, follows_src,
-                                           gcur, sbytes);
-    countS<<<dim3(NBUCK, 3), 256, 0, stream>>>(sbytes, gbase, scales);
-    fillB2<<<dim3(NBUCK, 3), 256, 0, stream>>>(pairs, gbase, row_ptr, scales, col);
-
-    const int* rp0 = row_ptr;                 const int* cl0 = col;
-    const int* rp1 = row_ptr + (N + 1);       const int* cl1 = col + E;
-    const int* rp2 = row_ptr + 2 * (N + 1);   const int* cl2 = col + 2 * (size_t)E;
-    const float* s_rates_out   = scales;
-    const float* s_rates_in    = scales + N;
-    const float* s_ratedby_out = scales + 2 * N;
-    const float* s_ratedby_in  = scales + 3 * N;
-    const float* s_follows_out = scales + 4 * N;
-    const float* s_follows_in  = scales + 5 * N;
-
-    const int GB128 = 384;
-    const int GB64  = 256;
-    const int SB128 = (N / 2 + 3) / 4;
-    const int SB64  = (N / 2 + 7) / 8;
-
-    gemm_mfma<128, float><<<GB128, 256, 0, stream>>>(feat_A, s_rates_out, Wt1_rates, T);
-    spmm128<false, true><<<SB128, 256, 0, stream>>>(rp0, cl0, T, s_rates_in,
-                                                    b1_rates, hB, N);
-    gemm_mfma<128, float><<<GB128, 256, 0, stream>>>(feat_B, s_ratedby_out, Wt1_ratedby, T);
-    spmm128<false, false><<<SB128, 256, 0, stream>>>(rp1, cl1, T, s_ratedby_in,
-                                                     b1_ratedby, hA, N);
-    gemm_mfma<128, float><<<GB128, 256, 0, stream>>>(feat_A, s_follows_out, Wt1_follows, T);
-    spmm128<true, true><<<SB128, 256, 0, stream>>>(rp2, cl2, T, s_follows_in,
-                                                   b1_follows, hA, N);
-
-    gemm_mfma<64, __half><<<GB64, 256, 0, stream>>>(hA, s_rates_out, Wt2_rates, T);
-    spmm64<false><<<SB64, 256, 0, stream>>>(rp0, cl0, T, s_rates_in, b2_rates, oB, N);
-    gemm_mfma<64, __half><<<GB64, 256, 0, stream>>>(hB, s_ratedby_out, Wt2_ratedby, T);
-    spmm64<false><<<SB64, 256, 0, stream>>>(rp1, cl1, T, s_ratedby_in, b2_ratedby, oA, N);
-    gemm_mfma<64, __half><<<GB64, 256, 0, stream>>>(hA, s_follows_out, Wt2_follows, T);
-    spmm64<true><<<SB64, 256, 0, stream>>>(rp2, cl2, T, s_follows_in, b2_follows, oA, N);
-
-    float* outp = (float*)d_out;
-    score_kernel<<<8192, 256, 0, stream>>>(oA, oB, rates_src, rates_dst, outp, E);
-    score_kernel<<<8192, 256, 0, stream>>>(oA, oB, neg_src, neg_dst, outp + E, E);
-}
+
+    fused0<<<6 * HB + 96, 256, 0, stream>>>(W1_rates, W1_ratedby, W1_follows,
+                                            W2_rates, W2_ratedby, W2_follows, Wt,
+                                            rates_src, rates_dst, ratedby_src,
+                                            ratedby_dst, follows_src, follows_dst,
+                                            bphist);
+    bucket_scan_par<<<6, 256, 0, stream>>>(bphist, gbase, gcur);
+    fused_bin<<<dim3(256, 6), 256, 0, stream>>>(rates_src, rates_dst, ratedby_src,
+                                                ratedby_dst, follows_src, follows_dst,
+                                                gcur, pairs, sbytes);
+    fused_finish<<<dim3(NBUCK, 6), 256, 0, stream>>>(pairs, sbytes, gbase,
+                                                     row_ptr, scales, col);
+
+    gemm_l1<<<3 * GB1, 256, 0, stream>>>(feat_A, feat_B, scales, Wt, T012);
+    spmm_l1<<<(3 * N / 2) / 4, 256, 0, stream>>>(row_ptr, col, T012, scales,
+                                                 b1_rates, b1_ratedby, b1_follows,
+                                                 hB, hA);
+    gemm_l2<<<3 * GB2, 256, 0, stream>>>(hA, hB, scales, Wt, Tp);
+    spmm_l2<<<(3 * N / 2) / 8, 256, 0, stream>>>(row_ptr, col, Tp, scales,
+                                                 b2_rates, b2_ratedby, b2_follows,
+                                                 oB, oA);
+    score2<<<8192, 256, 0, stream>>>(oA, oB, rates_src, rates_dst,
+                                     neg_src, neg_dst, (float*)d_out);
+}
```

Measured after the change: 358.9 us. 1.24x faster.
